# Kernel tuning notes

Hardware: AMD Instinct MI355X
Metric: run time of the kernel (lower is better)

Reference implementation:

```python
import jax, jax.numpy as jnp
import numpy as np


def setup_inputs() -> dict:
    key = jax.random.key(0)
    k1, k2 = jax.random.split(key)
    inp = jax.random.normal(k1, (32, 1, 128, 128), dtype=jnp.float32)
    mask = (jax.random.uniform(k2, (32, 1, 1, 128)) < 0.25).astype(jnp.float32)
    return {"input": inp, "mask": mask}


def reference(input, mask):
    # Faithful to KSpaceMap.forward: `mask` is accepted but never used there.
    # Original: k = RFFT(x) (unnormalized full 2D FFT via torch.rfft onesided=False),
    # repeat W times, zero all but column i, then IFFT2 (torch.ifft, includes 1/(H*W)),
    # keep the real channel -> out[b, i, h, w].
    # Because the mask is a one-hot frequency column, ifft2 factorizes analytically:
    #   ifft2(onehot_col_i(k)) = (1/W) * ifft_h(k)[:, i] outer exp(2*pi*j*i*w/W)
    # which avoids materializing the [B, W, 2, H, W] repeated k-space.
    B, _, H, W = input.shape
    x = input[:, 0, :, :]                              # [B, H, W]
    k = jnp.fft.fft2(x)                                # [B, H, W] complex, unnormalized FFT
    A = jnp.fft.ifft(k, axis=-2)                       # ifft over height (1/H included): [B, H, W]
    w = jnp.arange(W)
    phase = 2.0 * jnp.pi * jnp.outer(w, w).astype(jnp.float32) / W   # [W(i), W(w)]
    Pr = jnp.cos(phase) / W                            # real part of DFT basis / W
    Pi = jnp.sin(phase) / W                            # imag part of DFT basis / W
    # out[b, i, h, w] = Re(A[b, h, i] * P[i, w])
    out = (jnp.einsum('bhi,iw->bihw', A.real.astype(jnp.float32), Pr)
           - jnp.einsum('bhi,iw->bihw', A.imag.astype(jnp.float32), Pi))
    return out
```

## Files before the change

kernel.cpp:

```cpp
#include <hip/hip_runtime.h>
#include <math.h>


typedef float f32x4 __attribute__((ext_vector_type(4)));

__global__ __launch_bounds__(256) void kspace_v3(const float* __restrict__ x,
                                                 float* __restrict__ out) {
    const int blk  = blockIdx.x;
    const int b    = blk / 33;
    const int g    = blk % 33;
    const int t    = threadIdx.x;
    const int wv   = t >> 6;
    const int lane = t & 63;
    const int hh0  = lane >> 1;
    const int h    = wv * 32 + hh0;
    const int half = lane & 1;

    const float* xp = x + ((size_t)b * 128 + h) * 128 + half * 64;
    float xs[64];
#pragma unroll
    for (int j = 0; j < 16; ++j) {
        const f32x4 v = ((const f32x4*)xp)[j];
        xs[4 * j + 0] = v.x;
        xs[4 * j + 1] = v.y;
        xs[4 * j + 2] = v.z;
        xs[4 * j + 3] = v.w;
    }

    const int nb = (g < 32) ? 2 : 1;
#pragma unroll 1
    for (int ib = 0; ib < nb; ++ib) {
        const int i = (g < 32) ? (g * 2 + ib) : 64;

        float sstep, cstep;
        sincospif((float)i * (1.0f / 64.0f), &sstep, &cstep);
        const float dc = cstep, ds = -sstep;

        float ar = 0.0f, aiv = 0.0f;
#pragma unroll
        for (int ch = 0; ch < 2; ++ch) {
            const int u0 = half * 64 + ch * 32;
            const int a0 = (i * u0) & 127;
            float s0, c0;
            sincospif((float)a0 * (1.0f / 64.0f), &s0, &c0);
            float cr = c0, ci = -s0;
#pragma unroll
            for (int j2 = 0; j2 < 32; ++j2) {
                const float xv = xs[ch * 32 + j2];
                ar  = fmaf(xv, cr, ar);
                aiv = fmaf(xv, ci, aiv);
                const float ncr = fmaf(cr, dc, -ci * ds);
                ci = fmaf(cr, ds, ci * dc);
                cr = ncr;
            }
        }
        ar  += __shfl_xor(ar, 1);
        aiv += __shfl_xor(aiv, 1);
        ar  *= (1.0f / 128.0f);
        aiv *= (1.0f / 128.0f);

        const int wbase = (lane & 31) * 4;
        float cwv[4], swv[4];
#pragma unroll
        for (int c = 0; c < 4; ++c) {
            const int k = (i * (wbase + c)) & 127;
            sincospif((float)k * (1.0f / 64.0f), &swv[c], &cwv[c]);
        }

        f32x4* const o1 = (f32x4*)out + (size_t)(b * 128 + i) * 4096;
        f32x4* const o2 = (f32x4*)out + (size_t)(b * 128 + (128 - i)) * 4096;
        const bool dup = (i >= 1 && i <= 63);

#pragma unroll
        for (int j = 0; j < 16; ++j) {
            const int hhl = (lane >> 5) + 2 * j;
            const int src = 2 * hhl;
            const float a  = __shfl(ar,  src);
            const float bb = __shfl(aiv, src);
            f32x4 v;
            v.x = fmaf(a, cwv[0], -bb * swv[0]);
            v.y = fmaf(a, cwv[1], -bb * swv[1]);
            v.z = fmaf(a, cwv[2], -bb * swv[2]);
            v.w = fmaf(a, cwv[3], -bb * swv[3]);
            const int idx = (wv * 32 + hhl) * 32 + (lane & 31);
            __builtin_nontemporal_store(v, &o1[idx]);
            if (dup) __builtin_nontemporal_store(v, &o2[idx]);
        }
    }
}

extern "C" void kernel_launch(void* const* d_in, const int* in_sizes, int n_in,
                              void* d_out, int out_size, void* d_ws, size_t ws_size,
                              hipStream_t stream) {
    const float* x = (const float*)d_in[0];
    float* out = (float*)d_out;
    kspace_v3<<<dim3(1056), dim3(256), 0, stream>>>(x, out);
}
```

Before: 59.51 us.

## Use shared-memory twiddle table and stage row DFT results in LDS

Replaces the per-thread recurrence twiddles and repeated sincospif calls with a 128-entry cos/sin table in shared memory. The row DFT results now go to LDS, so the write phase reads them from there instead of using cross-lane shuffles. The grid shrinks from 33 to 32 blocks per batch, with the last block also handling column 64. Stores become regular instead of nontemporal, and the launch bound asks for 4 blocks per CU. This trades arithmetic and transcendental work for LDS lookups with possible bank conflicts, gives the last block one extra column, and may change cache behaviour on the large output write.

```diff
diff --git a/kernel.cpp b/kernel.cpp
--- a/kernel.cpp
+++ b/kernel.cpp
@@ -4,17 +4,26 @@
 
 typedef float f32x4 __attribute__((ext_vector_type(4)));
 
-__global__ __launch_bounds__(256) void kspace_v3(const float* __restrict__ x,
-                                                 float* __restrict__ out) {
+__global__ __launch_bounds__(256, 4) void kspace_v4(const float* __restrict__ x,
+                                                    float* __restrict__ out) {
     const int blk  = blockIdx.x;
-    const int b    = blk / 33;
-    const int g    = blk % 33;
+    const int b    = blk >> 5;
+    const int g    = blk & 31;
     const int t    = threadIdx.x;
     const int wv   = t >> 6;
     const int lane = t & 63;
-    const int hh0  = lane >> 1;
-    const int h    = wv * 32 + hh0;
+    const int h    = wv * 32 + (lane >> 1);
     const int half = lane & 1;
+
+    __shared__ __align__(16) float ct[128], st[128];
+    __shared__ __align__(16) float arL[3][128], aiL[3][128];
+
+    if (t < 128) {
+        float s, c;
+        sincospif((float)t * (1.0f / 64.0f), &s, &c);
+        ct[t] = c;
+        st[t] = s;
+    }
 
     const float* xp = x + ((size_t)b * 128 + h) * 128 + half * 64;
     float xs[64];
@@ -26,45 +35,42 @@
         xs[4 * j + 2] = v.z;
         xs[4 * j + 3] = v.w;
     }
+    __syncthreads();
 
-    const int nb = (g < 32) ? 2 : 1;
+    const int nI = (g == 31) ? 3 : 2;
+
 #pragma unroll 1
-    for (int ib = 0; ib < nb; ++ib) {
-        const int i = (g < 32) ? (g * 2 + ib) : 64;
-
-        float sstep, cstep;
-        sincospif((float)i * (1.0f / 64.0f), &sstep, &cstep);
-        const float dc = cstep, ds = -sstep;
-
+    for (int ii = 0; ii < nI; ++ii) {
+        const int i = g * 2 + ii;
         float ar = 0.0f, aiv = 0.0f;
+        const int u0 = half * 64;
 #pragma unroll
-        for (int ch = 0; ch < 2; ++ch) {
-            const int u0 = half * 64 + ch * 32;
-            const int a0 = (i * u0) & 127;
-            float s0, c0;
-            sincospif((float)a0 * (1.0f / 64.0f), &s0, &c0);
-            float cr = c0, ci = -s0;
-#pragma unroll
-            for (int j2 = 0; j2 < 32; ++j2) {
-                const float xv = xs[ch * 32 + j2];
-                ar  = fmaf(xv, cr, ar);
-                aiv = fmaf(xv, ci, aiv);
-                const float ncr = fmaf(cr, dc, -ci * ds);
-                ci = fmaf(cr, ds, ci * dc);
-                cr = ncr;
-            }
+        for (int j = 0; j < 64; ++j) {
+            const int k = (i * (u0 + j)) & 127;
+            const float xv = xs[j];
+            ar  = fmaf(xv,  ct[k], ar);
+            aiv = fmaf(xv, -st[k], aiv);
         }
         ar  += __shfl_xor(ar, 1);
         aiv += __shfl_xor(aiv, 1);
-        ar  *= (1.0f / 128.0f);
-        aiv *= (1.0f / 128.0f);
+        if (half == 0) {
+            arL[ii][h] = ar  * (1.0f / 128.0f);
+            aiL[ii][h] = aiv * (1.0f / 128.0f);
+        }
+    }
+    __syncthreads();
+
+#pragma unroll 1
+    for (int ii = 0; ii < nI; ++ii) {
+        const int i = g * 2 + ii;
 
         const int wbase = (lane & 31) * 4;
         float cwv[4], swv[4];
 #pragma unroll
         for (int c = 0; c < 4; ++c) {
             const int k = (i * (wbase + c)) & 127;
-            sincospif((float)k * (1.0f / 64.0f), &swv[c], &cwv[c]);
+            cwv[c] = ct[k];
+            swv[c] = st[k];
         }
 
         f32x4* const o1 = (f32x4*)out + (size_t)(b * 128 + i) * 4096;
@@ -73,18 +79,17 @@
 
 #pragma unroll
         for (int j = 0; j < 16; ++j) {
-            const int hhl = (lane >> 5) + 2 * j;
-            const int src = 2 * hhl;
-            const float a  = __shfl(ar,  src);
-            const float bb = __shfl(aiv, src);
+            const int q  = t + j * 256;
+            const int hh = q >> 5;
+            const float a  = arL[ii][hh];
+            const float bb = aiL[ii][hh];
             f32x4 v;
             v.x = fmaf(a, cwv[0], -bb * swv[0]);
             v.y = fmaf(a, cwv[1], -bb * swv[1]);
             v.z = fmaf(a, cwv[2], -bb * swv[2]);
             v.w = fmaf(a, cwv[3], -bb * swv[3]);
-            const int idx = (wv * 32 + hhl) * 32 + (lane & 31);
-            __builtin_nontemporal_store(v, &o1[idx]);
-            if (dup) __builtin_nontemporal_store(v, &o2[idx]);
+            o1[q] = v;
+            if (dup) o2[q] = v;
         }
     }
 }
@@ -94,5 +99,5 @@
                               hipStream_t stream) {
     const float* x = (const float*)d_in[0];
     float* out = (float*)d_out;
-    kspace_v3<<<dim3(1056), dim3(256), 0, stream>>>(x, out);
+    kspace_v4<<<dim3(1024), dim3(256), 0, stream>>>(x, out);
 }
```

Result: slower. 64.54 us (+8.5%).

## Rebalance grid to 1024 blocks and compute next plane's DFT after stores

Applied to the files above, without the earlier changes.

Plane 64 is no longer handled by its own extra block. The g==0 block of each batch now takes it as a third plane, so the grid shrinks to 1024 blocks with no tail block. The DFT reduction for the next plane is moved after the current plane's stores, so arithmetic can overlap with outstanding writes. Mirror planes are written in a separate pass with normal (not nontemporal) stores, and the store indexing is now contiguous per wave. The risk is that one block per batch does extra work, and dropping the nontemporal hint may change cache behaviour.

```diff
diff --git a/kernel.cpp b/kernel.cpp
--- a/kernel.cpp
+++ b/kernel.cpp
@@ -4,16 +4,44 @@
 
 typedef float f32x4 __attribute__((ext_vector_type(4)));
 
-__global__ __launch_bounds__(256) void kspace_v3(const float* __restrict__ x,
+__device__ __forceinline__ void dft_plane(const float* xs, int i, int half,
+                                          float& arO, float& aiO) {
+    float sstep, cstep;
+    sincospif((float)i * (1.0f / 64.0f), &sstep, &cstep);
+    const float dc = cstep, ds = -sstep;
+    float ar = 0.0f, ai = 0.0f;
+#pragma unroll
+    for (int ch = 0; ch < 2; ++ch) {
+        const int u0 = half * 64 + ch * 32;
+        const int a0 = (i * u0) & 127;
+        float s0, c0;
+        sincospif((float)a0 * (1.0f / 64.0f), &s0, &c0);
+        float cr = c0, ci = -s0;
+#pragma unroll
+        for (int j2 = 0; j2 < 32; ++j2) {
+            const float xv = xs[ch * 32 + j2];
+            ar = fmaf(xv, cr, ar);
+            ai = fmaf(xv, ci, ai);
+            const float ncr = fmaf(cr, dc, -ci * ds);
+            ci = fmaf(cr, ds, ci * dc);
+            cr = ncr;
+        }
+    }
+    ar += __shfl_xor(ar, 1);
+    ai += __shfl_xor(ai, 1);
+    arO = ar * (1.0f / 128.0f);
+    aiO = ai * (1.0f / 128.0f);
+}
+
+__global__ __launch_bounds__(256) void kspace_v6(const float* __restrict__ x,
                                                  float* __restrict__ out) {
     const int blk  = blockIdx.x;
-    const int b    = blk / 33;
-    const int g    = blk % 33;
+    const int b    = blk >> 5;
+    const int g    = blk & 31;
     const int t    = threadIdx.x;
     const int wv   = t >> 6;
     const int lane = t & 63;
-    const int hh0  = lane >> 1;
-    const int h    = wv * 32 + hh0;
+    const int h    = wv * 32 + (lane >> 1);
     const int half = lane & 1;
 
     const float* xp = x + ((size_t)b * 128 + h) * 128 + half * 64;
@@ -27,37 +55,14 @@
         xs[4 * j + 3] = v.w;
     }
 
-    const int nb = (g < 32) ? 2 : 1;
+    const int nP = (g == 0) ? 3 : 2;
+
+    float arC, aiC;
+    dft_plane(xs, 2 * g, half, arC, aiC);
+
 #pragma unroll 1
-    for (int ib = 0; ib < nb; ++ib) {
-        const int i = (g < 32) ? (g * 2 + ib) : 64;
-
-        float sstep, cstep;
-        sincospif((float)i * (1.0f / 64.0f), &sstep, &cstep);
-        const float dc = cstep, ds = -sstep;
-
-        float ar = 0.0f, aiv = 0.0f;
-#pragma unroll
-        for (int ch = 0; ch < 2; ++ch) {
-            const int u0 = half * 64 + ch * 32;
-            const int a0 = (i * u0) & 127;
-            float s0, c0;
-            sincospif((float)a0 * (1.0f / 64.0f), &s0, &c0);
-            float cr = c0, ci = -s0;
-#pragma unroll
-            for (int j2 = 0; j2 < 32; ++j2) {
-                const float xv = xs[ch * 32 + j2];
-                ar  = fmaf(xv, cr, ar);
-                aiv = fmaf(xv, ci, aiv);
-                const float ncr = fmaf(cr, dc, -ci * ds);
-                ci = fmaf(cr, ds, ci * dc);
-                cr = ncr;
-            }
-        }
-        ar  += __shfl_xor(ar, 1);
-        aiv += __shfl_xor(aiv, 1);
-        ar  *= (1.0f / 128.0f);
-        aiv *= (1.0f / 128.0f);
+    for (int p = 0; p < nP; ++p) {
+        const int i = (p < 2) ? (2 * g + p) : 64;
 
         const int wbase = (lane & 31) * 4;
         float cwv[4], swv[4];
@@ -67,24 +72,31 @@
             sincospif((float)k * (1.0f / 64.0f), &swv[c], &cwv[c]);
         }
 
-        f32x4* const o1 = (f32x4*)out + (size_t)(b * 128 + i) * 4096;
-        f32x4* const o2 = (f32x4*)out + (size_t)(b * 128 + (128 - i)) * 4096;
-        const bool dup = (i >= 1 && i <= 63);
+        const int npass = (i == 0 || i == 64) ? 1 : 2;
+#pragma unroll 1
+        for (int pass = 0; pass < npass; ++pass) {
+            const int pl = pass ? (128 - i) : i;
+            f32x4* const o = (f32x4*)out + (size_t)(b * 128 + pl) * 4096;
+#pragma unroll
+            for (int j = 0; j < 16; ++j) {
+                const int src = 4 * j + 2 * (lane >> 5);
+                const float a  = __shfl(arC, src);
+                const float bb = __shfl(aiC, src);
+                f32x4 v;
+                v.x = fmaf(a, cwv[0], -bb * swv[0]);
+                v.y = fmaf(a, cwv[1], -bb * swv[1]);
+                v.z = fmaf(a, cwv[2], -bb * swv[2]);
+                v.w = fmaf(a, cwv[3], -bb * swv[3]);
+                o[wv * 1024 + j * 64 + lane] = v;
+            }
+        }
 
-#pragma unroll
-        for (int j = 0; j < 16; ++j) {
-            const int hhl = (lane >> 5) + 2 * j;
-            const int src = 2 * hhl;
-            const float a  = __shfl(ar,  src);
-            const float bb = __shfl(aiv, src);
-            f32x4 v;
-            v.x = fmaf(a, cwv[0], -bb * swv[0]);
-            v.y = fmaf(a, cwv[1], -bb * swv[1]);
-            v.z = fmaf(a, cwv[2], -bb * swv[2]);
-            v.w = fmaf(a, cwv[3], -bb * swv[3]);
-            const int idx = (wv * 32 + hhl) * 32 + (lane & 31);
-            __builtin_nontemporal_store(v, &o1[idx]);
-            if (dup) __builtin_nontemporal_store(v, &o2[idx]);
+        if (p + 1 < nP) {
+            const int inext = (p + 1 < 2) ? (2 * g + p + 1) : 64;
+            float arN, aiN;
+            dft_plane(xs, inext, half, arN, aiN);
+            arC = arN;
+            aiC = aiN;
         }
     }
 }
@@ -94,5 +106,5 @@
                               hipStream_t stream) {
     const float* x = (const float*)d_in[0];
     float* out = (float*)d_out;
-    kspace_v3<<<dim3(1056), dim3(256), 0, stream>>>(x, out);
+    kspace_v6<<<dim3(1024), dim3(256), 0, stream>>>(x, out);
 }
```

Result: faster. 49.76 us (median of 2 runs) (-16.4%).
